# Kernel tuning notes

Hardware: AMD Instinct MI355X
Metric: run time of the kernel (lower is better)

## Reference

```python
import jax, jax.numpy as jnp
import numpy as np

N = 200000   # total nodes across batched graphs
E = 800000   # total edges
B = 4096     # number of graphs
IN = 32      # node feature dim
H1 = 128
D = 64       # set2set / conv3 dim


def setup_inputs():
    key = jax.random.key(0)
    ks = jax.random.split(key, 36)
    def rn(k, shape, s=0.05):
        return jax.random.normal(k, shape, dtype=jnp.float32) * s
    inp = {}
    inp["x"] = jax.random.normal(ks[0], (N, IN), dtype=jnp.float32)
    inp["edge_attr"] = jax.random.uniform(ks[1], (E, 6), dtype=jnp.float32)
    inp["t"] = jax.random.uniform(ks[2], (B, 1), dtype=jnp.float32)
    inp["p"] = jax.random.uniform(ks[3], (B, 1), dtype=jnp.float32)
    inp["e1_w"] = rn(ks[4], (6, IN));    inp["e1_b"] = rn(ks[5], (IN,))
    inp["nn1_w"] = rn(ks[6], (IN, H1));  inp["nn1_b"] = rn(ks[7], (H1,))
    inp["l1_w"] = rn(ks[8], (IN, H1));   inp["l1_b"] = rn(ks[9], (H1,))
    inp["e2_w"] = rn(ks[10], (6, H1));   inp["e2_b"] = rn(ks[11], (H1,))
    inp["nn2_w"] = rn(ks[12], (H1, H1)); inp["nn2_b"] = rn(ks[13], (H1,))
    inp["l2_w"] = rn(ks[14], (H1, H1));  inp["l2_b"] = rn(ks[15], (H1,))
    inp["e3_w"] = rn(ks[16], (6, H1));   inp["e3_b"] = rn(ks[17], (H1,))
    inp["nn3_w"] = rn(ks[18], (H1, D));  inp["nn3_b"] = rn(ks[19], (D,))
    inp["l3_w"] = rn(ks[20], (H1, D));   inp["l3_b"] = rn(ks[21], (D,))
    inp["lstm_wih"] = rn(ks[22], (2 * D, 4 * D))
    inp["lstm_whh"] = rn(ks[23], (D, 4 * D))
    inp["lstm_bih"] = rn(ks[24], (4 * D,))
    inp["lstm_bhh"] = rn(ks[25], (4 * D,))
    inp["l4_w"] = rn(ks[26], (2 * D + 2, H1)); inp["l4_b"] = rn(ks[27], (H1,))
    inp["l5_w"] = rn(ks[28], (H1, 1));         inp["l5_b"] = rn(ks[29], (1,))
    inp["edge_index"] = jax.random.randint(ks[30], (2, E), 0, N)
    inp["batch"] = jnp.sort(jax.random.randint(ks[31], (N,), 0, B))
    inp["num_graphs"] = B
    return inp


def _gine(x, edge_index, edge_attr, ew, eb, nw, nb):
    # PyG GINEConv with eps=0: nn((1+eps)*x_i + sum_j relu(x_j + edge_lin(e_ji)))
    src, dst = edge_index[0], edge_index[1]
    msg = jax.nn.relu(x[src] + edge_attr @ ew + eb)               # [E, d]
    aggr = jax.ops.segment_sum(msg, dst, num_segments=x.shape[0])  # [N, d]
    return (x + aggr) @ nw + nb


def _set2set(x, batch, num_graphs, wih, whh, bih, bhh, steps=3):
    d = x.shape[1]
    h = jnp.zeros((num_graphs, d), x.dtype)
    c = jnp.zeros((num_graphs, d), x.dtype)
    q_star = jnp.zeros((num_graphs, 2 * d), x.dtype)
    for _ in range(steps):
        # single-step LSTM (torch gate order i, f, g, o)
        gates = q_star @ wih + h @ whh + bih + bhh
        i, f, g, o = jnp.split(gates, 4, axis=1)
        c = jax.nn.sigmoid(f) * c + jax.nn.sigmoid(i) * jnp.tanh(g)
        h = jax.nn.sigmoid(o) * jnp.tanh(c)
        q = h
        # segment-wise softmax attention over nodes of each graph
        e = jnp.sum(x * q[batch], axis=1)                           # [N]
        emax = jax.ops.segment_max(e, batch, num_segments=num_graphs)
        a = jnp.exp(e - emax[batch])
        asum = jax.ops.segment_sum(a, batch, num_segments=num_graphs)
        a = a / asum[batch]
        r = jax.ops.segment_sum(a[:, None] * x, batch, num_segments=num_graphs)
        q_star = jnp.concatenate([q, r], axis=1)
    return q_star


def reference(x, edge_attr, t, p, e1_w, e1_b, nn1_w, nn1_b, l1_w, l1_b, e2_w, e2_b, nn2_w, nn2_b, l2_w, l2_b, e3_w, e3_b, nn3_w, nn3_b, l3_w, l3_b, lstm_wih, lstm_whh, lstm_bih, lstm_bhh, l4_w, l4_b, l5_w, l5_b, edge_index, batch, num_graphs):
    h = jax.nn.elu(_gine(x, edge_index, edge_attr, e1_w, e1_b, nn1_w, nn1_b) + x @ l1_w + l1_b)
    h = jax.nn.elu(_gine(h, edge_index, edge_attr, e2_w, e2_b, nn2_w, nn2_b) + h @ l2_w + l2_b)
    h = _gine(h, edge_index, edge_attr, e3_w, e3_b, nn3_w, nn3_b) + h @ l3_w + l3_b
    out = _set2set(h, batch, num_graphs, lstm_wih, lstm_whh, lstm_bih, lstm_bhh)
    out = jnp.concatenate([out, t, p], axis=1)  # [B, 130]
    out = jax.nn.relu(out @ l4_w + l4_b)
    out = out @ l5_w + l5_b
    return out.reshape(-1)
```

## Files before the change

### kernel.cpp

```cpp
#include <hip/hip_runtime.h>
#include <hip/hip_bf16.h>
#include <math.h>

#define DEV __device__ __forceinline__
using u16 = unsigned short;
typedef __attribute__((ext_vector_type(8))) short bf16x8;
typedef __attribute__((ext_vector_type(4))) float f32x4;

DEV float elu1(float x) { return x > 0.f ? x : expm1f(x); }
DEV float sigm(float x) { return 1.f / (1.f + expf(-x)); }
DEV float b2f(u16 v) { return __uint_as_float((unsigned)v << 16); }
DEV u16 f2b(float x) { __hip_bfloat16 b = __float2bfloat16(x); return *reinterpret_cast<u16*>(&b); }

__global__ __launch_bounds__(256) void deg_hist(const int* __restrict__ ei,
                                                int* __restrict__ deg, int E) {
    const int e = blockIdx.x * 256 + threadIdx.x;
    if (e < E) atomicAdd(&deg[ei[E + e]], 1);
}

__global__ __launch_bounds__(256) void scan1(const int* __restrict__ deg,
                                             int* __restrict__ part,
                                             int* __restrict__ bsum, int N) {
    __shared__ int lds[256];
    const int t = threadIdx.x;
    const int base = blockIdx.x * 1024;
    int v[4]; int s = 0;
    #pragma unroll
    for (int k = 0; k < 4; ++k) {
        const int idx = base + t * 4 + k;
        v[k] = (idx < N) ? deg[idx] : 0;
        s += v[k];
    }
    lds[t] = s; __syncthreads();
    int incl = s;
    for (int off = 1; off < 256; off <<= 1) {
        const int add = (t >= off) ? lds[t - off] : 0;
        __syncthreads();
        incl += add; lds[t] = incl;
        __syncthreads();
    }
    if (t == 255) bsum[blockIdx.x] = incl;
    int run = incl - s;
    #pragma unroll
    for (int k = 0; k < 4; ++k) {
        const int idx = base + t * 4 + k;
        if (idx < N) part[idx] = run;
        run += v[k];
    }
}

__global__ __launch_bounds__(256) void scan2(int* __restrict__ bsum, int nb) {
    __shared__ int lds[256];
    __shared__ int carry;
    const int t = threadIdx.x;
    if (t == 0) carry = 0;
    __syncthreads();
    for (int base = 0; base < nb; base += 256) {
        const int idx = base + t;
        const int v = (idx < nb) ? bsum[idx] : 0;
        lds[t] = v; __syncthreads();
        int incl = v;
        for (int off = 1; off < 256; off <<= 1) {
            const int add = (t >= off) ? lds[t - off] : 0;
            __syncthreads();
            incl += add; lds[t] = incl;
            __syncthreads();
        }
        const int c = carry;
        if (idx < nb) bsum[idx] = c + incl - v;
        __syncthreads();
        if (t == 255) carry = c + incl;
        __syncthreads();
    }
}

__global__ __launch_bounds__(256) void scan3(const int* __restrict__ part,
                                             const int* __restrict__ bsum,
                                             int* __restrict__ rowstart,
                                             int* __restrict__ cursor, int N, int E) {
    const int i = blockIdx.x * 256 + threadIdx.x;
    if (i < N) {
        const int v = part[i] + bsum[i >> 10];
        rowstart[i] = v;
        cursor[i] = v;
    }
    if (i == 0) rowstart[N] = E;
}

__global__ __launch_bounds__(256) void edge_scatter(const int* __restrict__ ei,
                                                    const float* __restrict__ eattr,
                                                    int* __restrict__ cursor,
                                                    int* __restrict__ src_s,
                                                    float* __restrict__ eattr_s, int E) {
    const int e = blockIdx.x * 256 + threadIdx.x;
    if (e >= E) return;
    const int src = ei[e], dst = ei[E + e];
    const float2 a0 = *(const float2*)(eattr + (size_t)e * 6);
    const float2 a1 = *(const float2*)(eattr + (size_t)e * 6 + 2);
    const float2 a2 = *(const float2*)(eattr + (size_t)e * 6 + 4);
    const int pos = atomicAdd(&cursor[dst], 1);
    src_s[pos] = src;
    float* ds = eattr_s + (size_t)pos * 6;
    *(float2*)ds = a0; *(float2*)(ds + 2) = a1; *(float2*)(ds + 4) = a2;
}

__global__ __launch_bounds__(256) void build_gstart(const int* __restrict__ batch,
                                                    int* __restrict__ gstart, int N, int B) {
    const int i = blockIdx.x * 256 + threadIdx.x;
    if (i >= N) return;
    const int b = batch[i];
    if (i == 0) for (int g = 0; g <= b; ++g) gstart[g] = 0;
    else {
        const int pb = batch[i - 1];
        for (int g = pb + 1; g <= b; ++g) gstart[g] = i;
    }
    if (i == N - 1) for (int g = b + 1; g <= B; ++g) gstart[g] = N;
}

template<int DIN, int DOUT>
__global__ __launch_bounds__(256) void wcat_prep(
    const float* __restrict__ nnW, const float* __restrict__ lW,
    const float* __restrict__ nnB, const float* __restrict__ lB,
    u16* __restrict__ wswz, float* __restrict__ bcomb)
{
    constexpr int COLT = DOUT / 16;
    const int idx = blockIdx.x * 256 + threadIdx.x;
    if (idx < 2 * DIN * DOUT) {
        const int k = idx / DOUT, n = idx % DOUT;
        const float v = (k < DIN) ? nnW[k * DOUT + n]
                                  : nnW[(k - DIN) * DOUT + n] + lW[(k - DIN) * DOUT + n];
        const int kc = k >> 5, khi = (k >> 3) & 3, j = k & 7;
        const int ct = n >> 4, n16 = n & 15;
        wswz[(size_t)(((kc * COLT + ct) * 4 + khi) * 16 + n16) * 8 + j] = f2b(v);
    }
    if (idx < DOUT) bcomb[idx] = nnB[idx] + lB[idx];
}

__global__ __launch_bounds__(256) void f32_to_bf16v(const float* __restrict__ src,
                                                    u16* __restrict__ dst, int n4) {
    const int i = blockIdx.x * 256 + threadIdx.x;
    if (i >= n4) return;
    const float4 v = *(const float4*)(src + (size_t)i * 4);
    ushort4 u; u.x = f2b(v.x); u.y = f2b(v.y); u.z = f2b(v.z); u.w = f2b(v.w);
    *(ushort4*)(dst + (size_t)i * 4) = u;
}

template<int DIN, int DOUT, bool ELU, typename TOUT>
__global__ __launch_bounds__(256) void fused_layer(
    const float* __restrict__ xf,
    const u16* __restrict__ hb,
    const float* __restrict__ eattr_s, const float* __restrict__ ew, const float* __restrict__ eb,
    const int* __restrict__ rowstart, const int* __restrict__ src_s,
    const u16* __restrict__ wswz, const float* __restrict__ bcomb,
    TOUT* __restrict__ out, int N)
{
    constexpr int KC1  = DIN / 32;
    constexpr int KC_TOT = 2 * KC1;
    constexpr int COLT = DOUT / 16;
    constexpr int CTW  = COLT / 4;
    constexpr int ASTR = (DIN == 32) ? 80 : 272;
    __shared__ char ldsb[64 * 272];
    const int tid = threadIdx.x;
    const int nb  = blockIdx.x * 64;

    if constexpr (DIN == 32) {
        const int j = tid & 31;
        const float w0 = ew[j], w1 = ew[32 + j], w2 = ew[64 + j],
                    w3 = ew[96 + j], w4 = ew[128 + j], w5 = ew[160 + j];
        const float bj = eb[j];
        #pragma unroll 2
        for (int it = 0; it < 8; ++it) {
            const int nl = it * 8 + (tid >> 5);
            const int n = nb + nl;
            if (n < N) {
                const int s0 = rowstart[n], s1 = rowstart[n + 1];
                float accA = 0.f, accB = 0.f;
                int k = s0;
                for (; k + 4 <= s1; k += 4) {
                    int sr[4];
                    #pragma unroll
                    for (int u = 0; u < 4; ++u) sr[u] = src_s[k + u];
                    float xv[4]; float2 ea[4][3];
                    #pragma unroll
                    for (int u = 0; u < 4; ++u) {
                        xv[u] = xf[(size_t)sr[u] * 32 + j];
                        const float* ep = eattr_s + (size_t)(k + u) * 6;
                        ea[u][0] = *(const float2*)ep;
                        ea[u][1] = *(const float2*)(ep + 2);
                        ea[u][2] = *(const float2*)(ep + 4);
                    }
                    #pragma unroll
                    for (int u = 0; u < 4; ++u) {
                        float el = bj;
                        el = fmaf(ea[u][0].x, w0, el); el = fmaf(ea[u][0].y, w1, el);
                        el = fmaf(ea[u][1].x, w2, el); el = fmaf(ea[u][1].y, w3, el);
                        el = fmaf(ea[u][2].x, w4, el); el = fmaf(ea[u][2].y, w5, el);
                        const float m = fmaxf(xv[u] + el, 0.f);
                        if (u & 1) accB += m; else accA += m;
                    }
                }
                for (; k < s1; ++k) {
                    const int sr = src_s[k];
                    const float* ep = eattr_s + (size_t)k * 6;
                    float el = bj;
                    el = fmaf(ep[0], w0, el); el = fmaf(ep[1], w1, el);
                    el = fmaf(ep[2], w2, el); el = fmaf(ep[3], w3, el);
                    el = fmaf(ep[4], w4, el); el = fmaf(ep[5], w5, el);
                    accA += fmaxf(xf[(size_t)sr * 32 + j] + el, 0.f);
                }
                *(u16*)(ldsb + nl * 80 + j * 2) = f2b(accA + accB);
            }
        }
    } else {
        const int lane = tid & 63;
        const int wid  = tid >> 6;
        const int j0 = lane << 1;
        float2 wv[6];
        #pragma unroll
        for (int q = 0; q < 6; ++q) wv[q] = *(const float2*)(ew + q * 128 + j0);
        const float2 bv = *(const float2*)(eb + j0);
        for (int it = 0; it < 16; ++it) {
            const int n = __builtin_amdgcn_readfirstlane(nb + it * 4 + wid);
            const int nl = n - nb;
            if (n < N) {
                const int s0 = rowstart[n], s1 = rowstart[n + 1];
                float a0A = 0.f, a1A = 0.f, a0B = 0.f, a1B = 0.f;
                int k = s0;
                for (; k + 4 <= s1; k += 4) {
                    int sr[4];
                    #pragma unroll
                    for (int u = 0; u < 4; ++u) sr[u] = src_s[k + u];
                    ushort2 xv[4];
                    #pragma unroll
                    for (int u = 0; u < 4; ++u)
                        xv[u] = *(const ushort2*)(hb + (size_t)sr[u] * 128 + j0);
                    #pragma unroll
                    for (int u = 0; u < 4; ++u) {
                        const float* ep = eattr_s + (size_t)(k + u) * 6;
                        const float e0 = ep[0], e1 = ep[1], e2 = ep[2],
                                    e3 = ep[3], e4 = ep[4], e5 = ep[5];
                        float l0 = bv.x, l1 = bv.y;
                        l0 = fmaf(e0, wv[0].x, l0); l1 = fmaf(e0, wv[0].y, l1);
                        l0 = fmaf(e1, wv[1].x, l0); l1 = fmaf(e1, wv[1].y, l1);
                        l0 = fmaf(e2, wv[2].x, l0); l1 = fmaf(e2, wv[2].y, l1);
                        l0 = fmaf(e3, wv[3].x, l0); l1 = fmaf(e3, wv[3].y, l1);
                        l0 = fmaf(e4, wv[4].x, l0); l1 = fmaf(e4, wv[4].y, l1);
                        l0 = fmaf(e5, wv[5].x, l0); l1 = fmaf(e5, wv[5].y, l1);
                        const float m0 = fmaxf(b2f(xv[u].x) + l0, 0.f);
                        const float m1 = fmaxf(b2f(xv[u].y) + l1, 0.f);
                        if (u & 1) { a0B += m0; a1B += m1; } else { a0A += m0; a1A += m1; }
                    }
                }
                for (; k < s1; ++k) {
                    const int sr = src_s[k];
                    const ushort2 xv = *(const ushort2*)(hb + (size_t)sr * 128 + j0);
                    const float* ep = eattr_s + (size_t)k * 6;
                    float l0 = bv.x, l1 = bv.y;
                    l0 = fmaf(ep[0], wv[0].x, l0); l1 = fmaf(ep[0], wv[0].y, l1);
                    l0 = fmaf(ep[1], wv[1].x, l0); l1 = fmaf(ep[1], wv[1].y, l1);
                    l0 = fmaf(ep[2], wv[2].x, l0); l1 = fmaf(ep[2], wv[2].y, l1);
                    l0 = fmaf(ep[3], wv[3].x, l0); l1 = fmaf(ep[3], wv[3].y, l1);
                    l0 = fmaf(ep[4], wv[4].x, l0); l1 = fmaf(ep[4], wv[4].y, l1);
                    l0 = fmaf(ep[5], wv[5].x, l0); l1 = fmaf(ep[5], wv[5].y, l1);
                    a0A += fmaxf(b2f(xv.x) + l0, 0.f);
                    a1A += fmaxf(b2f(xv.y) + l1, 0.f);
                }
                ushort2 o; o.x = f2b(a0A + a0B); o.y = f2b(a1A + a1B);
                *(ushort2*)(ldsb + nl * 272 + j0 * 2) = o;
            }
        }
    }
    __syncthreads();

    const int lane = tid & 63, wid = tid >> 6;
    const int n16 = lane & 15, khi = lane >> 4;
    f32x4 acc[4][CTW];
    #pragma unroll
    for (int g = 0; g < 4; ++g)
        #pragma unroll
        for (int c = 0; c < CTW; ++c) acc[g][c] = (f32x4){0.f, 0.f, 0.f, 0.f};
    #pragma unroll
    for (int kc = 0; kc < KC_TOT; ++kc) {
        bf16x8 bf[CTW];
        #pragma unroll
        for (int c = 0; c < CTW; ++c) {
            const int ct = wid * CTW + c;
            bf[c] = *(const bf16x8*)(wswz + (size_t)(((kc * COLT + ct) * 4 + khi) * 16 + n16) * 8);
        }
        #pragma unroll
        for (int g = 0; g < 4; ++g) {
            bf16x8 af;
            if (kc < KC1) {
                af = *(const bf16x8*)(ldsb + (g * 16 + n16) * ASTR + kc * 64 + khi * 16);
            } else {
                const int row = min(nb + g * 16 + n16, N - 1);
                af = *(const bf16x8*)(hb + (size_t)row * DIN + (kc - KC1) * 32 + khi * 8);
            }
            #pragma unroll
            for (int c = 0; c < CTW; ++c)
                acc[g][c] = __builtin_amdgcn_mfma_f32_16x16x32_bf16(af, bf[c], acc[g][c], 0, 0, 0);
        }
    }
    __syncthreads();

    #pragma unroll
    for (int c = 0; c < CTW; ++c) {
        const int col = (wid * CTW + c) * 16 + n16;
        const float bv = bcomb[col];
        #pragma unroll
        for (int g = 0; g < 4; ++g) {
            #pragma unroll
            for (int r = 0; r < 4; ++r) {
                const int nl = g * 16 + khi * 4 + r;
                float v = acc[g][c][r] + bv;
                if (ELU) v = elu1(v);
                if constexpr (sizeof(TOUT) == 2) *(u16*)(ldsb + nl * 272 + col * 2) = f2b(v);
                else                             *(float*)(ldsb + nl * 272 + col * 4) = v;
            }
        }
    }
    __syncthreads();
    char* outc = (char*)out;
    #pragma unroll
    for (int it = 0; it < 4; ++it) {
        const int task = it * 256 + tid;
        const int row = task >> 4, cch = task & 15;
        if (nb + row < N)
            *(float4*)(outc + (size_t)(nb + row) * (DOUT * sizeof(TOUT)) + cch * 16) =
                *(const float4*)(ldsb + row * 272 + cch * 16);
    }
}

__global__ __launch_bounds__(256) void lstm_gates(
    const float* __restrict__ qstar, const float* __restrict__ hS,
    const float* __restrict__ wih, const float* __restrict__ whh,
    const float* __restrict__ bih, const float* __restrict__ bhh,
    float* __restrict__ gates, int B)
{
    const int idx = blockIdx.x * 256 + threadIdx.x;
    const int g = idx >> 8, jj = idx & 255;
    if (g >= B) return;
    float acc = bih[jj] + bhh[jj];
    const float* q = qstar + g * 128;
    const float* h = hS + g * 64;
    #pragma unroll 4
    for (int k = 0; k < 128; ++k) acc = fmaf(q[k], wih[k * 256 + jj], acc);
    #pragma unroll 4
    for (int k = 0; k < 64;  ++k) acc = fmaf(h[k], whh[k * 256 + jj], acc);
    gates[g * 256 + jj] = acc;
}

__global__ __launch_bounds__(256) void lstm_update(
    const float* __restrict__ gates, float* __restrict__ cS, float* __restrict__ hS, int B)
{
    const int idx = blockIdx.x * 256 + threadIdx.x;
    const int g = idx >> 6, d = idx & 63;
    if (g >= B) return;
    const float i_ = gates[g * 256 + d];
    const float f_ = gates[g * 256 + 64 + d];
    const float g_ = gates[g * 256 + 128 + d];
    const float o_ = gates[g * 256 + 192 + d];
    float c = cS[g * 64 + d];
    c = sigm(f_) * c + sigm(i_) * tanhf(g_);
    cS[g * 64 + d] = c;
    hS[g * 64 + d] = sigm(o_) * tanhf(c);
}

__global__ __launch_bounds__(256) void attn_step(
    const float* __restrict__ h3, const float* __restrict__ hS,
    const int* __restrict__ gstart, float* __restrict__ qstar, int B)
{
    const int g = (blockIdx.x * 256 + threadIdx.x) >> 6;
    const int lane = threadIdx.x & 63;
    if (g >= B) return;
    const float q = hS[g * 64 + lane];
    const int s0 = gstart[g], s1 = gstart[g + 1];
    float m = -INFINITY, ssum = 0.f, racc = 0.f;
    int n = s0;
    for (; n + 2 <= s1; n += 2) {
        const float hv0 = h3[(size_t)n * 64 + lane];
        const float hv1 = h3[(size_t)(n + 1) * 64 + lane];
        float v0 = hv0 * q, v1 = hv1 * q;
        #pragma unroll
        for (int off = 32; off; off >>= 1) {
            v0 += __shfl_xor(v0, off, 64);
            v1 += __shfl_xor(v1, off, 64);
        }
        const float mnew = fmaxf(m, fmaxf(v0, v1));
        const float sc = expf(m - mnew);
        const float a0 = expf(v0 - mnew);
        const float a1 = expf(v1 - mnew);
        ssum = ssum * sc + a0 + a1;
        racc = racc * sc + a0 * hv0 + a1 * hv1;
        m = mnew;
    }
    for (; n < s1; ++n) {
        const float hv = h3[(size_t)n * 64 + lane];
        float v = hv * q;
        #pragma unroll
        for (int off = 32; off; off >>= 1) v += __shfl_xor(v, off, 64);
        const float mnew = fmaxf(m, v);
        const float sc = expf(m - mnew);
        const float a  = expf(v - mnew);
        ssum = ssum * sc + a;
        racc = racc * sc + a * hv;
        m = mnew;
    }
    const float r = (ssum > 0.f) ? racc / ssum : 0.f;
    qstar[g * 128 + lane] = q;
    qstar[g * 128 + 64 + lane] = r;
}

__global__ __launch_bounds__(256) void mlp_hidden(
    const float* __restrict__ qstar, const float* __restrict__ t, const float* __restrict__ p,
    const float* __restrict__ l4w, const float* __restrict__ l4b,
    float* __restrict__ hidden, int B)
{
    const int idx = blockIdx.x * 256 + threadIdx.x;
    const int g = idx >> 7, j = idx & 127;
    if (g >= B) return;
    float acc = l4b[j];
    const float* q = qstar + g * 128;
    #pragma unroll 4
    for (int k = 0; k < 128; ++k) acc = fmaf(q[k], l4w[k * 128 + j], acc);
    acc = fmaf(t[g], l4w[128 * 128 + j], acc);
    acc = fmaf(p[g], l4w[129 * 128 + j], acc);
    hidden[g * 128 + j] = fmaxf(acc, 0.f);
}

__global__ __launch_bounds__(256) void out_proj(
    const float* __restrict__ hidden, const float* __restrict__ l5w,
    const float* __restrict__ l5b, float* __restrict__ dout, int B)
{
    const int wid = (blockIdx.x * 256 + threadIdx.x) >> 6;
    const int lane = threadIdx.x & 63;
    if (wid >= B) return;
    float s = fmaf(hidden[wid * 128 + lane], l5w[lane],
                   hidden[wid * 128 + 64 + lane] * l5w[64 + lane]);
    #pragma unroll
    for (int m = 32; m; m >>= 1) s += __shfl_xor(s, m, 64);
    if (lane == 0) dout[wid] = s + l5b[0];
}

extern "C" void kernel_launch(void* const* d_in, const int* in_sizes, int n_in,
                              void* d_out, int out_size, void* d_ws, size_t ws_size,
                              hipStream_t stream)
{
    const float* x     = (const float*)d_in[0];
    const float* eattr = (const float*)d_in[1];
    const float* t     = (const float*)d_in[2];
    const float* p     = (const float*)d_in[3];
    const float* e1w = (const float*)d_in[4];  const float* e1b = (const float*)d_in[5];
    const float* nn1w= (const float*)d_in[6];  const float* nn1b= (const float*)d_in[7];
    const float* l1w = (const float*)d_in[8];  const float* l1b = (const float*)d_in[9];
    const float* e2w = (const float*)d_in[10]; const float* e2b = (const float*)d_in[11];
    const float* nn2w= (const float*)d_in[12]; const float* nn2b= (const float*)d_in[13];
    const float* l2w = (const float*)d_in[14]; const float* l2b = (const float*)d_in[15];
    const float* e3w = (const float*)d_in[16]; const float* e3b = (const float*)d_in[17];
    const float* nn3w= (const float*)d_in[18]; const float* nn3b= (const float*)d_in[19];
    const float* l3w = (const float*)d_in[20]; const float* l3b = (const float*)d_in[21];
    const float* wih = (const float*)d_in[22]; const float* whh = (const float*)d_in[23];
    const float* bih = (const float*)d_in[24]; const float* bhh = (const float*)d_in[25];
    const float* l4w = (const float*)d_in[26]; const float* l4b = (const float*)d_in[27];
    const float* l5w = (const float*)d_in[28]; const float* l5b = (const float*)d_in[29];
    const int* ei    = (const int*)d_in[30];
    const int* batch = (const int*)d_in[31];
    float* dout = (float*)d_out;

    const int N = in_sizes[0] / 32;
    const int E = in_sizes[30] / 2;
    const int B = in_sizes[2];

    char* basep = (char*)d_ws;
    size_t off = 0;
    auto take = [&](size_t bytes) -> char* {
        char* ptr = basep + off;
        off = (off + bytes + 255) & ~(size_t)255;
        return ptr;
    };
    int* src_s      = (int*)  take((size_t)E * 4);
    float* eattr_s  = (float*)take((size_t)E * 24);
    int* deg      = (int*) take((size_t)N * 4);
    int* part     = (int*) take((size_t)N * 4);
    int* bsum     = (int*) take(4096);
    int* rowstart = (int*) take((size_t)(N + 1) * 4);
    int* cursor   = (int*) take((size_t)N * 4);
    int* gstart   = (int*) take((size_t)(B + 1) * 4);
    u16* h1       = (u16*) take((size_t)N * 128 * 2);
    u16* h2       = (u16*) take((size_t)N * 128 * 2);
    float* h3     = (float*)h1;
    u16* xb       = (u16*) take((size_t)N * 32 * 2);
    u16* w1swz    = (u16*) take((size_t)2 * 32 * 128 * 2);
    u16* w2swz    = (u16*) take((size_t)2 * 128 * 128 * 2);
    u16* w3swz    = (u16*) take((size_t)2 * 128 * 64 * 2);
    float* b1c    = (float*)take(128 * 4);
    float* b2c    = (float*)take(128 * 4);
    float* b3c    = (float*)take(64 * 4);
    float* hS     = (float*)take((size_t)B * 256 * 4);
    float* cS     = hS + (size_t)B * 64;
    float* qstar  = cS + (size_t)B * 64;
    float* gates  = (float*)take((size_t)B * 256 * 4);
    float* hidden = (float*)take((size_t)B * 128 * 4);
    (void)ws_size;

    hipMemsetAsync(deg, 0, (size_t)N * 4, stream);
    deg_hist<<<(E + 255) / 256, 256, 0, stream>>>(ei, deg, E);
    const int NB1 = (N + 1023) / 1024;
    scan1<<<NB1, 256, 0, stream>>>(deg, part, bsum, N);
    scan2<<<1, 256, 0, stream>>>(bsum, NB1);
    scan3<<<(N + 255) / 256, 256, 0, stream>>>(part, bsum, rowstart, cursor, N, E);
    edge_scatter<<<(E + 255) / 256, 256, 0, stream>>>(ei, eattr, cursor, src_s, eattr_s, E);
    build_gstart<<<(N + 255) / 256, 256, 0, stream>>>(batch, gstart, N, B);
    f32_to_bf16v<<<(N * 8 + 255) / 256, 256, 0, stream>>>(x, xb, N * 8);
    wcat_prep<32, 128><<<(2 * 32 * 128 + 255) / 256, 256, 0, stream>>>(nn1w, l1w, nn1b, l1b, w1swz, b1c);
    wcat_prep<128, 128><<<(2 * 128 * 128 + 255) / 256, 256, 0, stream>>>(nn2w, l2w, nn2b, l2b, w2swz, b2c);
    wcat_prep<128, 64><<<(2 * 128 * 64 + 255) / 256, 256, 0, stream>>>(nn3w, l3w, nn3b, l3b, w3swz, b3c);

    const int FB = (N + 63) / 64;
    fused_layer<32, 128, true, u16><<<FB, 256, 0, stream>>>(
        x, xb, eattr_s, e1w, e1b, rowstart, src_s, w1swz, b1c, h1, N);
    fused_layer<128, 128, true, u16><<<FB, 256, 0, stream>>>(
        nullptr, h1, eattr_s, e2w, e2b, rowstart, src_s, w2swz, b2c, h2, N);
    fused_layer<128, 64, false, float><<<FB, 256, 0, stream>>>(
        nullptr, h2, eattr_s, e3w, e3b, rowstart, src_s, w3swz, b3c, h3, N);

    hipMemsetAsync(hS, 0, (size_t)B * 256 * 4, stream);
    for (int step = 0; step < 3; ++step) {
        lstm_gates<<<(B * 256 + 255) / 256, 256, 0, stream>>>(qstar, hS, wih, whh, bih, bhh, gates, B);
        lstm_update<<<(B * 64 + 255) / 256, 256, 0, stream>>>(gates, cS, hS, B);
        attn_step<<<(B * 64 + 255) / 256, 256, 0, stream>>>(h3, hS, gstart, qstar, B);
    }

    mlp_hidden<<<(B * 128 + 255) / 256, 256, 0, stream>>>(qstar, t, p, l4w, l4b, hidden, B);
    out_proj<<<(B * 64 + 255) / 256, 256, 0, stream>>>(hidden, l5w, l5b, dout, B);
}
```

Baseline: 645.6 us.

## Pair nodes per wave in edge gather and split set2set attention into node-parallel passes

```diff
diff --git a/kernel.cpp b/kernel.cpp
--- a/kernel.cpp
+++ b/kernel.cpp
@@ -11,6 +11,13 @@
 DEV float sigm(float x) { return 1.f / (1.f + expf(-x)); }
 DEV float b2f(u16 v) { return __uint_as_float((unsigned)v << 16); }
 DEV u16 f2b(float x) { __hip_bfloat16 b = __float2bfloat16(x); return *reinterpret_cast<u16*>(&b); }
+DEV unsigned fkey(float f) {
+    unsigned u = __float_as_uint(f);
+    return (u & 0x80000000u) ? ~u : (u | 0x80000000u);
+}
+DEV float funkey(unsigned u) {
+    return (u & 0x80000000u) ? __uint_as_float(u & 0x7fffffffu) : __uint_as_float(~u);
+}
 
 __global__ __launch_bounds__(256) void deg_hist(const int* __restrict__ ei,
                                                 int* __restrict__ deg, int E) {
@@ -147,8 +154,7 @@
 
 template<int DIN, int DOUT, bool ELU, typename TOUT>
 __global__ __launch_bounds__(256) void fused_layer(
-    const float* __restrict__ xf,
-    const u16* __restrict__ hb,
+    const float* __restrict__ xf, const u16* __restrict__ hb,
     const float* __restrict__ eattr_s, const float* __restrict__ ew, const float* __restrict__ eb,
     const int* __restrict__ rowstart, const int* __restrict__ src_s,
     const u16* __restrict__ wswz, const float* __restrict__ bcomb,
@@ -165,26 +171,24 @@
 
     if constexpr (DIN == 32) {
         const int j = tid & 31;
+        const int slot = tid >> 5;
         const float w0 = ew[j], w1 = ew[32 + j], w2 = ew[64 + j],
                     w3 = ew[96 + j], w4 = ew[128 + j], w5 = ew[160 + j];
         const float bj = eb[j];
-        #pragma unroll 2
         for (int it = 0; it < 8; ++it) {
-            const int nl = it * 8 + (tid >> 5);
-            const int n = nb + nl;
+            const int n = nb + it * 8 + slot;
             if (n < N) {
-                const int s0 = rowstart[n], s1 = rowstart[n + 1];
+                const int s0 = rowstart[n];
+                const int len = rowstart[n + 1] - s0;
                 float accA = 0.f, accB = 0.f;
-                int k = s0;
-                for (; k + 4 <= s1; k += 4) {
-                    int sr[4];
-                    #pragma unroll
-                    for (int u = 0; u < 4; ++u) sr[u] = src_s[k + u];
-                    float xv[4]; float2 ea[4][3];
+                for (int kk = 0; kk < len; kk += 4) {
+                    int ee[4]; float xv[4]; float2 ea[4][3];
+                    #pragma unroll
+                    for (int u = 0; u < 4; ++u) ee[u] = s0 + min(kk + u, len - 1);
                     #pragma unroll
                     for (int u = 0; u < 4; ++u) {
-                        xv[u] = xf[(size_t)sr[u] * 32 + j];
-                        const float* ep = eattr_s + (size_t)(k + u) * 6;
+                        xv[u] = xf[(size_t)src_s[ee[u]] * 32 + j];
+                        const float* ep = eattr_s + (size_t)ee[u] * 6;
                         ea[u][0] = *(const float2*)ep;
                         ea[u][1] = *(const float2*)(ep + 2);
                         ea[u][2] = *(const float2*)(ep + 4);
@@ -196,19 +200,11 @@
                         el = fmaf(ea[u][1].x, w2, el); el = fmaf(ea[u][1].y, w3, el);
                         el = fmaf(ea[u][2].x, w4, el); el = fmaf(ea[u][2].y, w5, el);
                         const float m = fmaxf(xv[u] + el, 0.f);
-                        if (u & 1) accB += m; else accA += m;
+                        const float mk = (kk + u < len) ? m : 0.f;
+                        if (u & 1) accB += mk; else accA += mk;
                     }
                 }
-                for (; k < s1; ++k) {
-                    const int sr = src_s[k];
-                    const float* ep = eattr_s + (size_t)k * 6;
-                    float el = bj;
-                    el = fmaf(ep[0], w0, el); el = fmaf(ep[1], w1, el);
-                    el = fmaf(ep[2], w2, el); el = fmaf(ep[3], w3, el);
-                    el = fmaf(ep[4], w4, el); el = fmaf(ep[5], w5, el);
-                    accA += fmaxf(xf[(size_t)sr * 32 + j] + el, 0.f);
-                }
-                *(u16*)(ldsb + nl * 80 + j * 2) = f2b(accA + accB);
+                *(u16*)(ldsb + (n - nb) * 80 + j * 2) = f2b(accA + accB);
             }
         }
     } else {
@@ -219,24 +215,36 @@
         #pragma unroll
         for (int q = 0; q < 6; ++q) wv[q] = *(const float2*)(ew + q * 128 + j0);
         const float2 bv = *(const float2*)(eb + j0);
-        for (int it = 0; it < 16; ++it) {
-            const int n = __builtin_amdgcn_readfirstlane(nb + it * 4 + wid);
-            const int nl = n - nb;
-            if (n < N) {
-                const int s0 = rowstart[n], s1 = rowstart[n + 1];
-                float a0A = 0.f, a1A = 0.f, a0B = 0.f, a1B = 0.f;
-                int k = s0;
-                for (; k + 4 <= s1; k += 4) {
-                    int sr[4];
-                    #pragma unroll
-                    for (int u = 0; u < 4; ++u) sr[u] = src_s[k + u];
-                    ushort2 xv[4];
+        for (int it = 0; it < 8; ++it) {
+            const int n0 = __builtin_amdgcn_readfirstlane(nb + it * 8 + wid * 2);
+            const int n1 = n0 + 1;
+            int sa = 0, la = 0, sb = 0, lb = 0;
+            if (n0 < N) { sa = rowstart[n0]; la = rowstart[n0 + 1] - sa; }
+            if (n1 < N) { sb = rowstart[n1]; lb = rowstart[n1 + 1] - sb; }
+            float a0 = 0.f, a1 = 0.f, b0 = 0.f, b1 = 0.f;
+            const int kmax = max(la, lb);
+            for (int kk = 0; kk < kmax; kk += 4) {
+                const bool ga = kk < la, gb = kk < lb;
+                int ea_[4], eb_[4];
+                ushort2 xva[4], xvb[4];
+                if (ga) {
+                    #pragma unroll
+                    for (int u = 0; u < 4; ++u) ea_[u] = sa + min(kk + u, la - 1);
                     #pragma unroll
                     for (int u = 0; u < 4; ++u)
-                        xv[u] = *(const ushort2*)(hb + (size_t)sr[u] * 128 + j0);
+                        xva[u] = *(const ushort2*)(hb + (size_t)src_s[ea_[u]] * 128 + j0);
+                }
+                if (gb) {
+                    #pragma unroll
+                    for (int u = 0; u < 4; ++u) eb_[u] = sb + min(kk + u, lb - 1);
+                    #pragma unroll
+                    for (int u = 0; u < 4; ++u)
+                        xvb[u] = *(const ushort2*)(hb + (size_t)src_s[eb_[u]] * 128 + j0);
+                }
+                if (ga) {
                     #pragma unroll
                     for (int u = 0; u < 4; ++u) {
-                        const float* ep = eattr_s + (size_t)(k + u) * 6;
+                        const float* ep = eattr_s + (size_t)ea_[u] * 6;
                         const float e0 = ep[0], e1 = ep[1], e2 = ep[2],
                                     e3 = ep[3], e4 = ep[4], e5 = ep[5];
                         float l0 = bv.x, l1 = bv.y;
@@ -246,28 +254,34 @@
                         l0 = fmaf(e3, wv[3].x, l0); l1 = fmaf(e3, wv[3].y, l1);
                         l0 = fmaf(e4, wv[4].x, l0); l1 = fmaf(e4, wv[4].y, l1);
                         l0 = fmaf(e5, wv[5].x, l0); l1 = fmaf(e5, wv[5].y, l1);
-                        const float m0 = fmaxf(b2f(xv[u].x) + l0, 0.f);
-                        const float m1 = fmaxf(b2f(xv[u].y) + l1, 0.f);
-                        if (u & 1) { a0B += m0; a1B += m1; } else { a0A += m0; a1A += m1; }
+                        const float m0 = fmaxf(b2f(xva[u].x) + l0, 0.f);
+                        const float m1 = fmaxf(b2f(xva[u].y) + l1, 0.f);
+                        if (kk + u < la) { a0 += m0; a1 += m1; }
                     }
                 }
-                for (; k < s1; ++k) {
-                    const int sr = src_s[k];
-                    const ushort2 xv = *(const ushort2*)(hb + (size_t)sr * 128 + j0);
-                    const float* ep = eattr_s + (size_t)k * 6;
-                    float l0 = bv.x, l1 = bv.y;
-                    l0 = fmaf(ep[0], wv[0].x, l0); l1 = fmaf(ep[0], wv[0].y, l1);
-                    l0 = fmaf(ep[1], wv[1].x, l0); l1 = fmaf(ep[1], wv[1].y, l1);
-                    l0 = fmaf(ep[2], wv[2].x, l0); l1 = fmaf(ep[2], wv[2].y, l1);
-                    l0 = fmaf(ep[3], wv[3].x, l0); l1 = fmaf(ep[3], wv[3].y, l1);
-                    l0 = fmaf(ep[4], wv[4].x, l0); l1 = fmaf(ep[4], wv[4].y, l1);
-                    l0 = fmaf(ep[5], wv[5].x, l0); l1 = fmaf(ep[5], wv[5].y, l1);
-                    a0A += fmaxf(b2f(xv.x) + l0, 0.f);
-                    a1A += fmaxf(b2f(xv.y) + l1, 0.f);
+                if (gb) {
+                    #pragma unroll
+                    for (int u = 0; u < 4; ++u) {
+                        const float* ep = eattr_s + (size_t)eb_[u] * 6;
+                        const float e0 = ep[0], e1 = ep[1], e2 = ep[2],
+                                    e3 = ep[3], e4 = ep[4], e5 = ep[5];
+                        float l0 = bv.x, l1 = bv.y;
+                        l0 = fmaf(e0, wv[0].x, l0); l1 = fmaf(e0, wv[0].y, l1);
+                        l0 = fmaf(e1, wv[1].x, l0); l1 = fmaf(e1, wv[1].y, l1);
+                        l0 = fmaf(e2, wv[2].x, l0); l1 = fmaf(e2, wv[2].y, l1);
+                        l0 = fmaf(e3, wv[3].x, l0); l1 = fmaf(e3, wv[3].y, l1);
+                        l0 = fmaf(e4, wv[4].x, l0); l1 = fmaf(e4, wv[4].y, l1);
+                        l0 = fmaf(e5, wv[5].x, l0); l1 = fmaf(e5, wv[5].y, l1);
+                        const float m0 = fmaxf(b2f(xvb[u].x) + l0, 0.f);
+                        const float m1 = fmaxf(b2f(xvb[u].y) + l1, 0.f);
+                        if (kk + u < lb) { b0 += m0; b1 += m1; }
+                    }
                 }
-                ushort2 o; o.x = f2b(a0A + a0B); o.y = f2b(a1A + a1B);
-                *(ushort2*)(ldsb + nl * 272 + j0 * 2) = o;
             }
+            if (n0 < N) { ushort2 o; o.x = f2b(a0); o.y = f2b(a1);
+                          *(ushort2*)(ldsb + (n0 - nb) * 272 + j0 * 2) = o; }
+            if (n1 < N) { ushort2 o; o.x = f2b(b0); o.y = f2b(b1);
+                          *(ushort2*)(ldsb + (n1 - nb) * 272 + j0 * 2) = o; }
         }
     }
     __syncthreads();
@@ -331,84 +345,93 @@
     }
 }
 
-__global__ __launch_bounds__(256) void lstm_gates(
-    const float* __restrict__ qstar, const float* __restrict__ hS,
+__global__ __launch_bounds__(256) void lstm_step(
+    const float* __restrict__ qstar,
     const float* __restrict__ wih, const float* __restrict__ whh,
     const float* __restrict__ bih, const float* __restrict__ bhh,
-    float* __restrict__ gates, int B)
-{
-    const int idx = blockIdx.x * 256 + threadIdx.x;
-    const int g = idx >> 8, jj = idx & 255;
-    if (g >= B) return;
-    float acc = bih[jj] + bhh[jj];
-    const float* q = qstar + g * 128;
-    const float* h = hS + g * 64;
-    #pragma unroll 4
-    for (int k = 0; k < 128; ++k) acc = fmaf(q[k], wih[k * 256 + jj], acc);
-    #pragma unroll 4
-    for (int k = 0; k < 64;  ++k) acc = fmaf(h[k], whh[k * 256 + jj], acc);
-    gates[g * 256 + jj] = acc;
-}
-
-__global__ __launch_bounds__(256) void lstm_update(
-    const float* __restrict__ gates, float* __restrict__ cS, float* __restrict__ hS, int B)
+    float* __restrict__ cS, float* __restrict__ hS,
+    unsigned* __restrict__ emaxu, int B)
 {
     const int idx = blockIdx.x * 256 + threadIdx.x;
     const int g = idx >> 6, d = idx & 63;
     if (g >= B) return;
-    const float i_ = gates[g * 256 + d];
-    const float f_ = gates[g * 256 + 64 + d];
-    const float g_ = gates[g * 256 + 128 + d];
-    const float o_ = gates[g * 256 + 192 + d];
-    float c = cS[g * 64 + d];
-    c = sigm(f_) * c + sigm(i_) * tanhf(g_);
-    cS[g * 64 + d] = c;
-    hS[g * 64 + d] = sigm(o_) * tanhf(c);
-}
-
-__global__ __launch_bounds__(256) void attn_step(
+    float ai = bih[d] + bhh[d];
+    float af = bih[64 + d] + bhh[64 + d];
+    float ag = bih[128 + d] + bhh[128 + d];
+    float ao = bih[192 + d] + bhh[192 + d];
+    const float* q = qstar + (size_t)g * 128;
+    const float* h = hS + (size_t)g * 64;
+    #pragma unroll 4
+    for (int k = 0; k < 128; ++k) {
+        const float qk = q[k];
+        const float* wr = wih + (size_t)k * 256;
+        ai = fmaf(qk, wr[d], ai);       af = fmaf(qk, wr[64 + d], af);
+        ag = fmaf(qk, wr[128 + d], ag); ao = fmaf(qk, wr[192 + d], ao);
+    }
+    #pragma unroll 4
+    for (int k = 0; k < 64; ++k) {
+        const float hk = h[k];
+        const float* wr = whh + (size_t)k * 256;
+        ai = fmaf(hk, wr[d], ai);       af = fmaf(hk, wr[64 + d], af);
+        ag = fmaf(hk, wr[128 + d], ag); ao = fmaf(hk, wr[192 + d], ao);
+    }
+    float c = cS[(size_t)g * 64 + d];
+    c = sigm(af) * c + sigm(ai) * tanhf(ag);
+    cS[(size_t)g * 64 + d] = c;
+    hS[(size_t)g * 64 + d] = sigm(ao) * tanhf(c);
+    if (d == 0) emaxu[g] = 0u;
+}
+
+__global__ __launch_bounds__(256) void attn_score(
     const float* __restrict__ h3, const float* __restrict__ hS,
-    const int* __restrict__ gstart, float* __restrict__ qstar, int B)
-{
-    const int g = (blockIdx.x * 256 + threadIdx.x) >> 6;
+    const int* __restrict__ batch, float* __restrict__ ebuf,
+    unsigned* __restrict__ emaxu, int N)
+{
+    int n = (blockIdx.x * 256 + threadIdx.x) >> 6;
     const int lane = threadIdx.x & 63;
+    n = __builtin_amdgcn_readfirstlane(n);
+    if (n >= N) return;
+    const int g = batch[n];
+    float v = h3[(size_t)n * 64 + lane] * hS[(size_t)g * 64 + lane];
+    #pragma unroll
+    for (int off = 32; off; off >>= 1) v += __shfl_xor(v, off, 64);
+    if (lane == 0) { ebuf[n] = v; atomicMax(&emaxu[g], fkey(v)); }
+}
+
+__global__ __launch_bounds__(256) void attn_finish(
+    const float* __restrict__ h3, const float* __restrict__ hS,
+    const int* __restrict__ gstart, const float* __restrict__ ebuf,
+    const unsigned* __restrict__ emaxu, float* __restrict__ qstar, int B)
+{
+    int g = (blockIdx.x * 256 + threadIdx.x) >> 6;
+    const int lane = threadIdx.x & 63;
+    g = __builtin_amdgcn_readfirstlane(g);
     if (g >= B) return;
-    const float q = hS[g * 64 + lane];
+    const float m = funkey(emaxu[g]);
     const int s0 = gstart[g], s1 = gstart[g + 1];
-    float m = -INFINITY, ssum = 0.f, racc = 0.f;
+    float ssum = 0.f, racc = 0.f;
     int n = s0;
-    for (; n + 2 <= s1; n += 2) {
-        const float hv0 = h3[(size_t)n * 64 + lane];
-        const float hv1 = h3[(size_t)(n + 1) * 64 + lane];
-        float v0 = hv0 * q, v1 = hv1 * q;
-        #pragma unroll
-        for (int off = 32; off; off >>= 1) {
-            v0 += __shfl_xor(v0, off, 64);
-            v1 += __shfl_xor(v1, off, 64);
-        }
-        const float mnew = fmaxf(m, fmaxf(v0, v1));
-        const float sc = expf(m - mnew);
-        const float a0 = expf(v0 - mnew);
-        const float a1 = expf(v1 - mnew);
-        ssum = ssum * sc + a0 + a1;
-        racc = racc * sc + a0 * hv0 + a1 * hv1;
-        m = mnew;
+    for (; n + 4 <= s1; n += 4) {
+        const float a0 = expf(ebuf[n] - m);
+        const float a1 = expf(ebuf[n + 1] - m);
+        const float a2 = expf(ebuf[n + 2] - m);
+        const float a3 = expf(ebuf[n + 3] - m);
+        const float r0 = h3[(size_t)n * 64 + lane];
+        const float r1 = h3[(size_t)(n + 1) * 64 + lane];
+        const float r2 = h3[(size_t)(n + 2) * 64 + lane];
+        const float r3 = h3[(size_t)(n + 3) * 64 + lane];
+        ssum += (a0 + a1) + (a2 + a3);
+        racc = fmaf(a0, r0, racc); racc = fmaf(a1, r1, racc);
+        racc = fmaf(a2, r2, racc); racc = fmaf(a3, r3, racc);
     }
     for (; n < s1; ++n) {
-        const float hv = h3[(size_t)n * 64 + lane];
-        float v = hv * q;
-        #pragma unroll
-        for (int off = 32; off; off >>= 1) v += __shfl_xor(v, off, 64);
-        const float mnew = fmaxf(m, v);
-        const float sc = expf(m - mnew);
-        const float a  = expf(v - mnew);
-        ssum = ssum * sc + a;
-        racc = racc * sc + a * hv;
-        m = mnew;
-    }
-    const float r = (ssum > 0.f) ? racc / ssum : 0.f;
-    qstar[g * 128 + lane] = q;
-    qstar[g * 128 + 64 + lane] = r;
+        const float a = expf(ebuf[n] - m);
+        ssum += a;
+        racc = fmaf(a, h3[(size_t)n * 64 + lane], racc);
+    }
+    const float q = hS[(size_t)g * 64 + lane];
+    qstar[(size_t)g * 128 + lane] = q;
+    qstar[(size_t)g * 128 + 64 + lane] = (ssum > 0.f) ? racc / ssum : 0.f;
 }
 
 __global__ __launch_bounds__(256) void mlp_hidden(
@@ -420,12 +443,12 @@
     const int g = idx >> 7, j = idx & 127;
     if (g >= B) return;
     float acc = l4b[j];
-    const float* q = qstar + g * 128;
+    const float* q = qstar + (size_t)g * 128;
     #pragma unroll 4
     for (int k = 0; k < 128; ++k) acc = fmaf(q[k], l4w[k * 128 + j], acc);
     acc = fmaf(t[g], l4w[128 * 128 + j], acc);
     acc = fmaf(p[g], l4w[129 * 128 + j], acc);
-    hidden[g * 128 + j] = fmaxf(acc, 0.f);
+    hidden[(size_t)g * 128 + j] = fmaxf(acc, 0.f);
 }
 
 __global__ __launch_bounds__(256) void out_proj(
@@ -435,8 +458,8 @@
     const int wid = (blockIdx.x * 256 + threadIdx.x) >> 6;
     const int lane = threadIdx.x & 63;
     if (wid >= B) return;
-    float s = fmaf(hidden[wid * 128 + lane], l5w[lane],
-                   hidden[wid * 128 + 64 + lane] * l5w[64 + lane]);
+    float s = fmaf(hidden[(size_t)wid * 128 + lane], l5w[lane],
+                   hidden[(size_t)wid * 128 + 64 + lane] * l5w[64 + lane]);
     #pragma unroll
     for (int m = 32; m; m >>= 1) s += __shfl_xor(s, m, 64);
     if (lane == 0) dout[wid] = s + l5b[0];
@@ -499,7 +522,8 @@
     float* hS     = (float*)take((size_t)B * 256 * 4);
     float* cS     = hS + (size_t)B * 64;
     float* qstar  = cS + (size_t)B * 64;
-    float* gates  = (float*)take((size_t)B * 256 * 4);
+    float* ebuf   = (float*)take((size_t)N * 4);
+    unsigned* emaxu = (unsigned*)take((size_t)B * 4);
     float* hidden = (float*)take((size_t)B * 128 * 4);
     (void)ws_size;
 
@@ -525,10 +549,11 @@
         nullptr, h2, eattr_s, e3w, e3b, rowstart, src_s, w3swz, b3c, h3, N);
 
     hipMemsetAsync(hS, 0, (size_t)B * 256 * 4, stream);
+    const int NWB = (N * 64 + 255) / 256;
     for (int step = 0; step < 3; ++step) {
-        lstm_gates<<<(B * 256 + 255) / 256, 256, 0, stream>>>(qstar, hS, wih, whh, bih, bhh, gates, B);
-        lstm_update<<<(B * 64 + 255) / 256, 256, 0, stream>>>(gates, cS, hS, B);
-        attn_step<<<(B * 64 + 255) / 256, 256, 0, stream>>>(h3, hS, gstart, qstar, B);
+        lstm_step<<<(B * 64 + 255) / 256, 256, 0, stream>>>(qstar, wih, whh, bih, bhh, cS, hS, emaxu, B);
+        attn_score<<<NWB, 256, 0, stream>>>(h3, hS, batch, ebuf, emaxu, N);
+        attn_finish<<<(B * 64 + 255) / 256, 256, 0, stream>>>(h3, hS, gstart, ebuf, emaxu, qstar, B);
     }
 
     mlp_hidden<<<(B * 128 + 255) / 256, 256, 0, stream>>>(qstar, t, p, l4w, l4b, hidden, B);
```

Result: slower. 786.1 us (+21.8%).
